# Performance work log

Hardware: AMD Instinct MI355X
Metric: run time of the kernel (lower is better)

The kernel has to match this reference:

```python
import jax, jax.numpy as jnp
import numpy as np
from jax import lax

B, CN, CL, CH = 8, 64, 32, 128
H, HM = 256, 512
DOWN, PAD, FW = 2, 5, 12
SLOPE = 0.2
GAIN = float(np.sqrt(2.0))
EPS = 1e-5


def setup_inputs() -> dict:
    key = jax.random.key(0)
    ks = jax.random.split(key, 8)
    # 12-tap separable lowpass FIR, normalized to unit DC gain (stylegan buffer)
    f1 = jnp.array([1, 3, 6, 10, 12, 14, 14, 12, 10, 6, 3, 1], jnp.float32)
    f1 = f1 / f1.sum()
    down_filter = jnp.outer(f1, f1)  # [12,12], separable 2D filter
    return {
        "x": jax.random.normal(ks[0], (B, CN, H, H), jnp.float32),
        "hm": jax.random.normal(ks[1], (B, CL, HM, HM), jnp.float32),
        "down_filter": down_filter,
        "w_shared": jax.random.normal(ks[2], (CH, CL), jnp.float32) * 0.1,
        "b_shared": jnp.zeros((CH,), jnp.float32),
        "w_gamma": jax.random.normal(ks[3], (CN, CH), jnp.float32) * 0.1,
        "b_gamma": jnp.zeros((CN,), jnp.float32),
        "w_beta": jax.random.normal(ks[4], (CN, CH), jnp.float32) * 0.1,
        "b_beta": jnp.zeros((CN,), jnp.float32),
    }


def _upfirdn2d_down(hm, f2d):
    # flip_filter=False in upfirdn2d: torch flips f then cross-correlates (=true conv).
    # XLA conv is cross-correlation, so flip the filter here too.
    f = jnp.flip(f2d, (0, 1))
    c = hm.shape[1]
    hm_p = jnp.pad(hm, ((0, 0), (0, 0), (PAD, PAD), (PAD, PAD)))
    k = jnp.broadcast_to(f[None, None], (c, 1, FW, FW))  # depthwise kernel
    return lax.conv_general_dilated(
        hm_p, k, window_strides=(DOWN, DOWN), padding="VALID",
        dimension_numbers=("NCHW", "OIHW", "NCHW"), feature_group_count=c)


def _conv1x1(t, w, b):
    return jnp.einsum("bchw,oc->bohw", t, w) + b[None, :, None, None]


def reference(x, hm, down_filter, w_shared, b_shared, w_gamma, b_gamma, w_beta, b_beta):
    # FIR downsample label map 512 -> 256
    hm_d = _upfirdn2d_down(hm, down_filter)
    # shared 1x1 conv + fused lrelu with gain (bias_act: act='lrelu', gain=sqrt(2))
    h = _conv1x1(hm_d, w_shared, b_shared)
    h = jnp.where(h >= 0, h, h * SLOPE) * GAIN
    gamma = _conv1x1(h, w_gamma, b_gamma)
    beta = _conv1x1(h, w_beta, b_beta)
    # InstanceNorm2d(affine=False): per (N,C) over HW, biased variance, eps=1e-5
    mu = jnp.mean(x, axis=(2, 3), keepdims=True)
    var = jnp.mean(jnp.square(x - mu), axis=(2, 3), keepdims=True)
    xn = (x - mu) * lax.rsqrt(var + EPS)
    return xn * (1.0 + gamma) + beta + 0.1 * x
```

## Files before the change

kernel.cpp:

```cpp
#include <hip/hip_runtime.h>
#include <cstdint>

typedef __bf16 bf16;
typedef bf16 bf16x4 __attribute__((ext_vector_type(4)));
typedef bf16 bf16x8 __attribute__((ext_vector_type(8)));
typedef float f32x4 __attribute__((ext_vector_type(4)));

__global__ __launch_bounds__(256) void k1_fused(const float* __restrict__ hm,
                                                const float* __restrict__ f2d,
                                                bf16* __restrict__ hmd) {
    __shared__ float in_t[42 * 144];
    __shared__ float v_t[16 * 144];
    __shared__ bf16  out_t[8 * 1024];

    const int tid = threadIdx.x;
    const int bid = blockIdx.x;
    const int xt = bid & 3;
    const int yt = (bid >> 2) & 15;
    const int b  = bid >> 6;
    const int y0 = yt * 16;
    const int x0 = xt * 64;
    const int R0 = 2 * y0 - 5;
    const int B0 = 2 * x0 - 8;

    float tv[12], th[12];
    const float inv = 1.0f / f2d[0];
#pragma unroll
    for (int j = 0; j < 12; ++j) { tv[j] = f2d[j * 12]; th[j] = f2d[j] * inv; }

    const float* srcb = hm + (size_t)b * 32 * 262144;

#pragma unroll 1
    for (int c = 0; c < 32; ++c) {
        const float* sc = srcb + (size_t)c * 262144;

#pragma unroll
        for (int k = 0; k < 6; ++k) {
            int idx = k * 256 + tid;
            if (idx < 1512) {
                int R = idx / 36;
                int q = idx - R * 36;
                int gr = R0 + R;
                int gc = B0 + 4 * q;
                f32x4 vv = {0.f, 0.f, 0.f, 0.f};
                if ((unsigned)gr < 512u && (unsigned)gc < 512u)
                    vv = *(const f32x4*)(sc + gr * 512 + gc);
                *(f32x4*)(in_t + R * 144 + 4 * q) = vv;
            }
        }
        __syncthreads();

#pragma unroll
        for (int s = 0; s < 2; ++s) {
            int idx = s * 256 + tid;
            if (idx < 288) {
                int yp = idx / 36;
                int q  = idx - yp * 36;
                const float* col = in_t + 4 * q;
                f32x4 a0 = {0.f, 0.f, 0.f, 0.f};
                f32x4 a1 = {0.f, 0.f, 0.f, 0.f};
#pragma unroll
                for (int r = 0; r < 14; ++r) {
                    f32x4 rv = *(const f32x4*)(col + (4 * yp + r) * 144);
                    if (r < 12)  a0 += tv[r] * rv;
                    if (r >= 2)  a1 += tv[r - 2] * rv;
                }
                *(f32x4*)(v_t + (2 * yp) * 144 + 4 * q) = a0;
                *(f32x4*)(v_t + (2 * yp + 1) * 144 + 4 * q) = a1;
            }
        }
        __syncthreads();

        bf16* oc = out_t + (c & 7) * 1024;
#pragma unroll
        for (int s = 0; s < 2; ++s) {
            int idx = s * 256 + tid;
            int yo = idx >> 5;
            int xp = idx & 31;
            int xo = 2 * xp;
            const float* vr = v_t + yo * 144 + 4 * xp + 3;
            float a0 = 0.f, a1 = 0.f;
#pragma unroll
            for (int r = 0; r < 14; ++r) {
                float vv = vr[r];
                if (r < 12)  a0 += th[r] * vv;
                if (r >= 2)  a1 += th[r - 2] * vv;
            }
            unsigned lo = __builtin_bit_cast(unsigned short, (bf16)a0);
            unsigned hi = __builtin_bit_cast(unsigned short, (bf16)a1);
            *(unsigned int*)(oc + yo * 64 + xo) = lo | (hi << 16);
        }

        if ((c & 7) == 7) {
            __syncthreads();
            int ph = c >> 3;
            const unsigned short* Ts = (const unsigned short*)out_t;
#pragma unroll
            for (int s = 0; s < 4; ++s) {
                int pix = s * 256 + tid;
                int yo = pix >> 6;
                int xo = pix & 63;
                unsigned int u[4];
#pragma unroll
                for (int g = 0; g < 4; ++g) {
                    unsigned lo = Ts[(2 * g) * 1024 + pix];
                    unsigned hi = Ts[(2 * g + 1) * 1024 + pix];
                    u[g] = lo | (hi << 16);
                }
                size_t p = ((size_t)(b * 256 + y0 + yo) * 256) + x0 + xo;
                *(uint4*)(hmd + p * 32 + ph * 8) = make_uint4(u[0], u[1], u[2], u[3]);
            }
        }
        __syncthreads();
    }
}

__global__ __launch_bounds__(256) void k0_prep(const float* __restrict__ w_shared,
                                               const float* __restrict__ w_gamma,
                                               const float* __restrict__ w_beta,
                                               bf16* __restrict__ wsb,
                                               bf16* __restrict__ wcat) {
    int t = blockIdx.x * 256 + threadIdx.x;
    if (t < 4096) wsb[t] = (bf16)w_shared[t];
    int n = t >> 7, k = t & 127;
    float wv = (n < 64) ? w_gamma[n * 128 + k] : w_beta[(n - 64) * 128 + k];
    wcat[t] = (bf16)wv;
}

__global__ __launch_bounds__(256) void k2_stats(const float* __restrict__ x,
                                                float* __restrict__ meanp,
                                                float* __restrict__ rstdp) {
    int bc = blockIdx.x;
    const float* p = x + (size_t)bc * 65536;
    int tid = threadIdx.x;
    float s = 0.f, s2 = 0.f;
#pragma unroll 4
    for (int i = 0; i < 64; ++i) {
        f32x4 vv = *(const f32x4*)(p + (i * 256 + tid) * 4);
        s += vv[0] + vv[1] + vv[2] + vv[3];
        s2 += vv[0] * vv[0] + vv[1] * vv[1] + vv[2] * vv[2] + vv[3] * vv[3];
    }
#pragma unroll
    for (int off = 32; off > 0; off >>= 1) {
        s += __shfl_down(s, off);
        s2 += __shfl_down(s2, off);
    }
    __shared__ float red[8];
    int w = tid >> 6, lane = tid & 63;
    if (lane == 0) { red[w] = s; red[4 + w] = s2; }
    __syncthreads();
    if (tid == 0) {
        float S = red[0] + red[1] + red[2] + red[3];
        float S2 = red[4] + red[5] + red[6] + red[7];
        float mu = S * (1.f / 65536.f);
        float var = S2 * (1.f / 65536.f) - mu * mu;
        meanp[bc] = mu;
        rstdp[bc] = rsqrtf(var + 1e-5f);
    }
}

__global__ __launch_bounds__(256) void k3_fused(
    const bf16* __restrict__ hmd, const bf16* __restrict__ wsb,
    const bf16* __restrict__ wcat, const float* __restrict__ bsh,
    const float* __restrict__ bga, const float* __restrict__ bbe,
    const float* __restrict__ x, const float* __restrict__ meanp,
    const float* __restrict__ rstdp, float* __restrict__ out) {
    constexpr int HROW = 136;
    __shared__ bf16 buf[4 * 4608];
    __shared__ float smean[64], srstd[64];

    const int tid = threadIdx.x;
    const int w = tid >> 6;
    const int lane = tid & 63;
    const int l15 = lane & 15;
    const int quad = lane >> 4;

    const int bid = blockIdx.x;
    const int b = bid >> 9;
    const int y = (bid >> 1) & 255;
    const int x0 = (bid & 1) << 7;

    if (tid < 64) {
        smean[tid] = meanp[b * 64 + tid];
        srstd[tid] = rstdp[b * 64 + tid];
    }

    bf16* Hw = buf + w * 4608;
    const int pw = bid * 128 + w * 32;

    bf16x8 a1[2];
#pragma unroll
    for (int mt = 0; mt < 2; ++mt)
        a1[mt] = *(const bf16x8*)(hmd + (size_t)(pw + mt * 16 + l15) * 32 + quad * 8);
    bf16x8 b1[8];
#pragma unroll
    for (int nt = 0; nt < 8; ++nt)
        b1[nt] = *(const bf16x8*)(wsb + (nt * 16 + l15) * 32 + quad * 8);
    f32x4 zero4 = {0.f, 0.f, 0.f, 0.f};
    f32x4 acc[2][8];
#pragma unroll
    for (int mt = 0; mt < 2; ++mt)
#pragma unroll
        for (int nt = 0; nt < 8; ++nt)
            acc[mt][nt] = __builtin_amdgcn_mfma_f32_16x16x32_bf16(a1[mt], b1[nt], zero4, 0, 0, 0);

#pragma unroll
    for (int nt = 0; nt < 8; ++nt) {
        float bs = bsh[nt * 16 + l15];
#pragma unroll
        for (int mt = 0; mt < 2; ++mt) {
#pragma unroll
            for (int r = 0; r < 4; ++r) {
                float hv = acc[mt][nt][r] + bs;
                hv = (hv >= 0.f ? hv : 0.2f * hv) * 1.41421356237309515f;
                int m = mt * 16 + quad * 4 + r;
                Hw[m * HROW + nt * 16 + l15] = (bf16)hv;
            }
        }
    }

    f32x4 acc2[2][8];
#pragma unroll
    for (int mt = 0; mt < 2; ++mt)
#pragma unroll
        for (int nt = 0; nt < 8; ++nt) acc2[mt][nt] = zero4;
#pragma unroll 1
    for (int kt = 0; kt < 4; ++kt) {
        bf16x8 b2[8];
#pragma unroll
        for (int nt = 0; nt < 8; ++nt)
            b2[nt] = *(const bf16x8*)(wcat + (nt * 16 + l15) * 128 + kt * 32 + quad * 8);
        bf16x8 a2[2];
#pragma unroll
        for (int mt = 0; mt < 2; ++mt)
            a2[mt] = *(const bf16x8*)(Hw + (mt * 16 + l15) * HROW + kt * 32 + quad * 8);
#pragma unroll
        for (int mt = 0; mt < 2; ++mt)
#pragma unroll
            for (int nt = 0; nt < 8; ++nt)
                acc2[mt][nt] = __builtin_amdgcn_mfma_f32_16x16x32_bf16(a2[mt], b2[nt], acc2[mt][nt], 0, 0, 0);
    }

#pragma unroll
    for (int nt = 0; nt < 8; ++nt) {
        int n = nt * 16 + l15;
        float bias = (n < 64) ? bga[n] : bbe[n - 64];
#pragma unroll
        for (int mt = 0; mt < 2; ++mt) {
            bf16x4 pk;
#pragma unroll
            for (int r = 0; r < 4; ++r) pk[r] = (bf16)(acc2[mt][nt][r] + bias);
            int m0 = mt * 16 + quad * 4;
            *(bf16x4*)(Hw + n * 36 + m0) = pk;
        }
    }
    __syncthreads();

    const size_t xbase = (size_t)b * 64 * 65536 + (size_t)y * 256 + x0;
#pragma unroll
    for (int it = 0; it < 8; ++it) {
        int g = it * 256 + tid;
        int c = g >> 5;
        int px = (g & 31) * 4;
        int wv = px >> 5, pm = px & 31;
        const bf16* GBv = buf + wv * 4608;
        bf16x4 gg = *(const bf16x4*)(GBv + c * 36 + pm);
        bf16x4 bb = *(const bf16x4*)(GBv + (c + 64) * 36 + pm);
        f32x4 xv = *(const f32x4*)(x + xbase + (size_t)c * 65536 + px);
        float mu = smean[c], rs = srstd[c];
        f32x4 o;
#pragma unroll
        for (int r = 0; r < 4; ++r) {
            float xn = (xv[r] - mu) * rs;
            o[r] = xn * (1.f + (float)gg[r]) + (float)bb[r] + 0.1f * xv[r];
        }
        *(f32x4*)(out + xbase + (size_t)c * 65536 + px) = o;
    }
}

extern "C" void kernel_launch(void* const* d_in, const int* in_sizes, int n_in,
                              void* d_out, int out_size, void* d_ws, size_t ws_size,
                              hipStream_t stream) {
    const float* x        = (const float*)d_in[0];
    const float* hm       = (const float*)d_in[1];
    const float* f2d      = (const float*)d_in[2];
    const float* w_shared = (const float*)d_in[3];
    const float* b_shared = (const float*)d_in[4];
    const float* w_gamma  = (const float*)d_in[5];
    const float* b_gamma  = (const float*)d_in[6];
    const float* w_beta   = (const float*)d_in[7];
    const float* b_beta   = (const float*)d_in[8];
    float* out = (float*)d_out;
    char* ws = (char*)d_ws;

    bf16*  hmd   = (bf16*)(ws + 0);
    bf16*  wsb   = (bf16*)(ws + 33554432);
    bf16*  wcat  = (bf16*)(ws + 33562624);
    float* meanp = (float*)(ws + 33595392);
    float* rstdp = (float*)(ws + 33597440);

    hipLaunchKernelGGL(k1_fused, dim3(512),  dim3(256), 0, stream, hm, f2d, hmd);
    hipLaunchKernelGGL(k0_prep,  dim3(64),   dim3(256), 0, stream, w_shared, w_gamma, w_beta, wsb, wcat);
    hipLaunchKernelGGL(k2_stats, dim3(512),  dim3(256), 0, stream, x, meanp, rstdp);
    hipLaunchKernelGGL(k3_fused, dim3(4096), dim3(256), 0, stream,
                       hmd, wsb, wcat, b_shared, b_gamma, b_beta, x, meanp, rstdp, out);
}
```

Baseline: 661.3 us.

## Split FIR downsample kernel across channel groups and smaller tiles for more blocks

The FIR downsample kernel now splits the 32 channels into 4 groups of 8 and uses 8-row output tiles, raising the grid from 512 to 4096 blocks. The intermediate bf16 map is stored as four channel-group planes, and the consumer kernel reads its MFMA A fragments from those planes. The LDS row pitch is padded to 148 to ease bank conflicts, and the horizontal pass loads its inputs as vectors into registers. The aim is better GPU occupancy and latency hiding. The cost is more halo re-reads, since smaller tiles reload the vertical filter overlap, and fewer threads are active in the vertical pass.

```diff
diff --git a/kernel.cpp b/kernel.cpp
--- a/kernel.cpp
+++ b/kernel.cpp
@@ -9,16 +9,18 @@
 __global__ __launch_bounds__(256) void k1_fused(const float* __restrict__ hm,
                                                 const float* __restrict__ f2d,
                                                 bf16* __restrict__ hmd) {
-    __shared__ float in_t[42 * 144];
-    __shared__ float v_t[16 * 144];
-    __shared__ bf16  out_t[8 * 1024];
+    constexpr int IR = 148;
+    __shared__ float in_t[26 * IR];
+    __shared__ float v_t[8 * IR];
+    __shared__ bf16  out_t[8 * 512];
 
     const int tid = threadIdx.x;
     const int bid = blockIdx.x;
-    const int xt = bid & 3;
-    const int yt = (bid >> 2) & 15;
-    const int b  = bid >> 6;
-    const int y0 = yt * 16;
+    const int cg = bid & 3;
+    const int xt = (bid >> 2) & 3;
+    const int yt = (bid >> 4) & 31;
+    const int b  = bid >> 9;
+    const int y0 = yt * 8;
     const int x0 = xt * 64;
     const int R0 = 2 * y0 - 5;
     const int B0 = 2 * x0 - 8;
@@ -28,16 +30,16 @@
 #pragma unroll
     for (int j = 0; j < 12; ++j) { tv[j] = f2d[j * 12]; th[j] = f2d[j] * inv; }
 
-    const float* srcb = hm + (size_t)b * 32 * 262144;
+    const float* srcb = hm + (size_t)(b * 32 + cg * 8) * 262144;
 
 #pragma unroll 1
-    for (int c = 0; c < 32; ++c) {
-        const float* sc = srcb + (size_t)c * 262144;
-
-#pragma unroll
-        for (int k = 0; k < 6; ++k) {
+    for (int ci = 0; ci < 8; ++ci) {
+        const float* sc = srcb + (size_t)ci * 262144;
+
+#pragma unroll
+        for (int k = 0; k < 4; ++k) {
             int idx = k * 256 + tid;
-            if (idx < 1512) {
+            if (idx < 936) {
                 int R = idx / 36;
                 int q = idx - R * 36;
                 int gr = R0 + R;
@@ -45,73 +47,67 @@
                 f32x4 vv = {0.f, 0.f, 0.f, 0.f};
                 if ((unsigned)gr < 512u && (unsigned)gc < 512u)
                     vv = *(const f32x4*)(sc + gr * 512 + gc);
-                *(f32x4*)(in_t + R * 144 + 4 * q) = vv;
+                *(f32x4*)(in_t + R * IR + 4 * q) = vv;
             }
         }
         __syncthreads();
 
-#pragma unroll
-        for (int s = 0; s < 2; ++s) {
-            int idx = s * 256 + tid;
-            if (idx < 288) {
-                int yp = idx / 36;
-                int q  = idx - yp * 36;
-                const float* col = in_t + 4 * q;
-                f32x4 a0 = {0.f, 0.f, 0.f, 0.f};
-                f32x4 a1 = {0.f, 0.f, 0.f, 0.f};
-#pragma unroll
-                for (int r = 0; r < 14; ++r) {
-                    f32x4 rv = *(const f32x4*)(col + (4 * yp + r) * 144);
-                    if (r < 12)  a0 += tv[r] * rv;
-                    if (r >= 2)  a1 += tv[r - 2] * rv;
-                }
-                *(f32x4*)(v_t + (2 * yp) * 144 + 4 * q) = a0;
-                *(f32x4*)(v_t + (2 * yp + 1) * 144 + 4 * q) = a1;
+        if (tid < 144) {
+            int yp = tid / 36;
+            int q  = tid - yp * 36;
+            const float* col = in_t + 4 * q;
+            f32x4 a0 = {0.f, 0.f, 0.f, 0.f};
+            f32x4 a1 = {0.f, 0.f, 0.f, 0.f};
+#pragma unroll
+            for (int r = 0; r < 14; ++r) {
+                f32x4 rv = *(const f32x4*)(col + (4 * yp + r) * IR);
+                if (r < 12)  a0 += tv[r] * rv;
+                if (r >= 2)  a1 += tv[r - 2] * rv;
             }
+            *(f32x4*)(v_t + (2 * yp) * IR + 4 * q) = a0;
+            *(f32x4*)(v_t + (2 * yp + 1) * IR + 4 * q) = a1;
         }
         __syncthreads();
 
-        bf16* oc = out_t + (c & 7) * 1024;
-#pragma unroll
-        for (int s = 0; s < 2; ++s) {
-            int idx = s * 256 + tid;
-            int yo = idx >> 5;
-            int xp = idx & 31;
-            int xo = 2 * xp;
-            const float* vr = v_t + yo * 144 + 4 * xp + 3;
+        {
+            int xp = tid & 31;
+            int yo = tid >> 5;
+            const float* vr4 = v_t + yo * IR + 4 * xp;
+            float arr[17];
+            *(f32x4*)(arr + 0)  = *(const f32x4*)(vr4 + 0);
+            *(f32x4*)(arr + 4)  = *(const f32x4*)(vr4 + 4);
+            *(f32x4*)(arr + 8)  = *(const f32x4*)(vr4 + 8);
+            *(f32x4*)(arr + 12) = *(const f32x4*)(vr4 + 12);
+            arr[16] = vr4[16];
             float a0 = 0.f, a1 = 0.f;
 #pragma unroll
-            for (int r = 0; r < 14; ++r) {
-                float vv = vr[r];
-                if (r < 12)  a0 += th[r] * vv;
-                if (r >= 2)  a1 += th[r - 2] * vv;
+            for (int r = 0; r < 12; ++r) {
+                a0 += th[r] * arr[3 + r];
+                a1 += th[r] * arr[5 + r];
             }
             unsigned lo = __builtin_bit_cast(unsigned short, (bf16)a0);
             unsigned hi = __builtin_bit_cast(unsigned short, (bf16)a1);
-            *(unsigned int*)(oc + yo * 64 + xo) = lo | (hi << 16);
-        }
-
-        if ((c & 7) == 7) {
-            __syncthreads();
-            int ph = c >> 3;
-            const unsigned short* Ts = (const unsigned short*)out_t;
-#pragma unroll
-            for (int s = 0; s < 4; ++s) {
-                int pix = s * 256 + tid;
-                int yo = pix >> 6;
-                int xo = pix & 63;
-                unsigned int u[4];
-#pragma unroll
-                for (int g = 0; g < 4; ++g) {
-                    unsigned lo = Ts[(2 * g) * 1024 + pix];
-                    unsigned hi = Ts[(2 * g + 1) * 1024 + pix];
-                    u[g] = lo | (hi << 16);
-                }
-                size_t p = ((size_t)(b * 256 + y0 + yo) * 256) + x0 + xo;
-                *(uint4*)(hmd + p * 32 + ph * 8) = make_uint4(u[0], u[1], u[2], u[3]);
-            }
+            *(unsigned int*)(out_t + ci * 512 + yo * 64 + 2 * xp) = lo | (hi << 16);
         }
         __syncthreads();
+    }
+
+    const unsigned short* Ts = (const unsigned short*)out_t;
+    bf16* plane = hmd + (size_t)cg * 4194304;
+#pragma unroll
+    for (int s = 0; s < 2; ++s) {
+        int pix = s * 256 + tid;
+        int yo = pix >> 6;
+        int xo = pix & 63;
+        unsigned int u[4];
+#pragma unroll
+        for (int g = 0; g < 4; ++g) {
+            unsigned lo = Ts[(2 * g) * 512 + pix];
+            unsigned hi = Ts[(2 * g + 1) * 512 + pix];
+            u[g] = lo | (hi << 16);
+        }
+        size_t p = ((size_t)(b * 256 + y0 + yo) * 256) + x0 + xo;
+        *(uint4*)(plane + p * 8) = make_uint4(u[0], u[1], u[2], u[3]);
     }
 }
 
@@ -188,10 +184,11 @@
     bf16* Hw = buf + w * 4608;
     const int pw = bid * 128 + w * 32;
 
+    const bf16* plane = hmd + (size_t)quad * 4194304;
     bf16x8 a1[2];
 #pragma unroll
     for (int mt = 0; mt < 2; ++mt)
-        a1[mt] = *(const bf16x8*)(hmd + (size_t)(pw + mt * 16 + l15) * 32 + quad * 8);
+        a1[mt] = *(const bf16x8*)(plane + (size_t)(pw + mt * 16 + l15) * 8);
     bf16x8 b1[8];
 #pragma unroll
     for (int nt = 0; nt < 8; ++nt)
@@ -299,7 +296,7 @@
     float* meanp = (float*)(ws + 33595392);
     float* rstdp = (float*)(ws + 33597440);
 
-    hipLaunchKernelGGL(k1_fused, dim3(512),  dim3(256), 0, stream, hm, f2d, hmd);
+    hipLaunchKernelGGL(k1_fused, dim3(4096), dim3(256), 0, stream, hm, f2d, hmd);
     hipLaunchKernelGGL(k0_prep,  dim3(64),   dim3(256), 0, stream, w_shared, w_gamma, w_beta, wsb, wcat);
     hipLaunchKernelGGL(k2_stats, dim3(512),  dim3(256), 0, stream, x, meanp, rstdp);
     hipLaunchKernelGGL(k3_fused, dim3(4096), dim3(256), 0, stream,
```

Measured after the change: 611.8 us. -7.5%, faster.
